# Kernel optimization log

Measured on AMD Instinct MI355X. Metric: run time of the kernel, lower is better.

The kernel has to match this reference:

```python
import jax, jax.numpy as jnp
import numpy as np

N_HEADS = 16
D_HEAD = 64
IGNORE = -100000.0


def setup_inputs() -> dict:
    key = jax.random.key(0)
    ks = jax.random.split(key, 5)
    B, S, D = 2, 2048, 1024
    return {
        "residual": jax.random.normal(ks[0], (B, S, D), dtype=jnp.float32),
        "q": jax.random.normal(ks[1], (B, S, D), dtype=jnp.float32),
        "k": jax.random.normal(ks[2], (B, S, D), dtype=jnp.float32),
        "v": jax.random.normal(ks[3], (B, S, D), dtype=jnp.float32),
        "W_O": jax.random.normal(ks[4], (N_HEADS, D_HEAD, D), dtype=jnp.float32) * 0.02,
        "b_O": jnp.zeros((D,), dtype=jnp.float32),
    }


def reference(residual, q, k, v, W_O, b_O):
    B, S, _ = q.shape
    attn_scale = np.sqrt(D_HEAD).astype(np.float32)  # use_attn_scale=True
    # split heads: [..., pos, (h d)] -> [..., pos, h, d]
    qh = q.reshape(B, S, N_HEADS, D_HEAD)
    kh = k.reshape(B, S, N_HEADS, D_HEAD)
    vh = v.reshape(B, S, N_HEADS, D_HEAD)
    # scores: [..., head, query_pos, key_pos]
    scores = jnp.einsum("bqhd,bkhd->bhqk", qh, kh) / attn_scale
    causal = jnp.tril(jnp.ones((S, S), dtype=bool))
    scores = jnp.where(causal, scores, jnp.float32(IGNORE))
    pattern = jax.nn.softmax(scores, axis=-1)
    # weighted sum of values: [..., query_pos, head, d_head]
    z = jnp.einsum("bkhd,bhqk->bqhd", vh, pattern)
    out = jnp.einsum("bqhd,hdm->bqm", z, W_O) + b_O
    return (residual, out)
```

## Files before the change

kernel.cpp:

```cpp
#include <hip/hip_runtime.h>

#define B_ 2
#define S_ 2048
#define D_ 1024
#define H_ 16
#define DH_ 64
#define NP_ 2048

typedef short v8s __attribute__((ext_vector_type(8)));
typedef float v4f __attribute__((ext_vector_type(4)));
typedef float v16f __attribute__((ext_vector_type(16)));
typedef unsigned int v2u __attribute__((ext_vector_type(2)));
typedef unsigned int uint32;

__device__ inline short f2bf(float f) {
  unsigned u = __float_as_uint(f);
  u = (u + 0x7FFFu + ((u >> 16) & 1u)) >> 16;
  return (short)u;
}

__device__ inline unsigned pk_bf16(float lo, float hi) {
  unsigned r;
  asm("v_cvt_pk_bf16_f32 %0, %1, %2" : "=v"(r) : "v"(lo), "v"(hi));
  return r;
}

__device__ inline void gll16(const void* g, void* l) {
  __builtin_amdgcn_global_load_lds(
      (const __attribute__((address_space(1))) void*)g,
      (__attribute__((address_space(3))) void*)l, 16, 0, 0);
}

__global__ __launch_bounds__(256) void cvt_all_kernel(
    const float* __restrict__ k, short* __restrict__ kb,
    const float* __restrict__ v, short* __restrict__ vt,
    const float* __restrict__ w, short* __restrict__ wt) {
  __shared__ short t[64][64 + 8];
  int bid = blockIdx.x;
  int tid = threadIdx.x;
  if (bid < 2048) {
    int i = bid * 256 + tid;
    float4 a = ((const float4*)k)[2 * i];
    float4 b = ((const float4*)k)[2 * i + 1];
    v8s o;
    o[0] = f2bf(a.x); o[1] = f2bf(a.y); o[2] = f2bf(a.z); o[3] = f2bf(a.w);
    o[4] = f2bf(b.x); o[5] = f2bf(b.y); o[6] = f2bf(b.z); o[7] = f2bf(b.w);
    ((v8s*)kb)[i] = o;
    return;
  }
  int r = tid >> 2, c16 = (tid & 3) * 16;
  if (bid < 3072) {
    int id = bid - 2048;
    int st = id & 31;
    int bh = id >> 5;
    int b = bh >> 4, h = bh & 15;
    const float* vp = v + ((size_t)(b * S_ + st * 64 + r)) * D_ + h * DH_ + c16;
    for (int i = 0; i < 16; i += 4) {
      float4 a = *(const float4*)(vp + i);
      t[r][c16 + i + 0] = f2bf(a.x);
      t[r][c16 + i + 1] = f2bf(a.y);
      t[r][c16 + i + 2] = f2bf(a.z);
      t[r][c16 + i + 3] = f2bf(a.w);
    }
    __syncthreads();
    short* op = vt + ((size_t)((b * H_ + h) * DH_ + r)) * S_ + st * 64 + c16;
    v8s o0, o1;
    for (int j = 0; j < 8; ++j) { o0[j] = t[c16 + j][r]; o1[j] = t[c16 + 8 + j][r]; }
    *(v8s*)op = o0;
    *(v8s*)(op + 8) = o1;
  } else {
    int id = bid - 3072;
    int tk = id & 15, tm = id >> 4;
    const float* wp = w + (size_t)(tk * 64 + r) * D_ + tm * 64 + c16;
    for (int i = 0; i < 16; i += 4) {
      float4 a = *(const float4*)(wp + i);
      t[r][c16 + i + 0] = f2bf(a.x);
      t[r][c16 + i + 1] = f2bf(a.y);
      t[r][c16 + i + 2] = f2bf(a.z);
      t[r][c16 + i + 3] = f2bf(a.w);
    }
    __syncthreads();
    short* op = wt + (size_t)(tm * 64 + r) * D_ + tk * 64 + c16;
    v8s o0, o1;
    for (int j = 0; j < 8; ++j) { o0[j] = t[c16 + j][r]; o1[j] = t[c16 + 8 + j][r]; }
    *(v8s*)op = o0;
    *(v8s*)(op + 8) = o1;
  }
}

template <int SPLITS>
__global__ __launch_bounds__(64, 4) void attn_kernel(
    const float* __restrict__ q, const short* __restrict__ kbf,
    const short* __restrict__ vtb, uint32* __restrict__ Opart,
    float* __restrict__ Lsum, const float* __restrict__ residual,
    float* __restrict__ res_out) {
  constexpr int NBLK = (SPLITS == 2) ? 4096 : 2048;
  int bid = blockIdx.x;
  int bh = bid & 31;
  int rest = bid >> 5;
  int sp = (SPLITS == 2) ? (rest & 1) : 0;
  int i = (SPLITS == 2) ? (rest >> 1) : rest;
  int b = bh >> 4, h = bh & 15;

  const int qrow0 = i * 32;
  const int nt = i + 1;
  const int t0 = (SPLITS == 2) ? sp * nt / 2 : 0;
  const int t1 = (SPLITS == 2) ? ((sp + 1) * nt / 2 - 1) : i;

  int lane = threadIdx.x;
  int l31 = lane & 31, h32 = lane >> 5;

  __shared__ short Klds[32][64];
  __shared__ short Vlds[32][64];

  const int lr8 = lane >> 3;
  const int l7 = lane & 7;
  const short* kbase = kbf + (size_t)b * S_ * D_ + h * DH_ +
                       (size_t)lr8 * D_ + ((l7 ^ lr8) << 3);
  const int vq = l7 ^ lr8;
  const short* vbase = vtb + (size_t)(b * H_ + h) * DH_ * S_ +
                       (size_t)(lr8 + (vq >> 2) * 32) * S_ + ((vq & 3) << 3);

  v8s qf[4];
  {
    const float* qp = q + (size_t)(b * S_ + qrow0 + l31) * D_ + h * DH_ + h32 * 8;
    const float sc = 0.125f * 1.44269504f;
#pragma unroll
    for (int d4 = 0; d4 < 4; ++d4) {
      float4 x = *(const float4*)(qp + d4 * 16);
      float4 y = *(const float4*)(qp + d4 * 16 + 4);
      v8s tq;
      tq[0] = f2bf(x.x * sc); tq[1] = f2bf(x.y * sc);
      tq[2] = f2bf(x.z * sc); tq[3] = f2bf(x.w * sc);
      tq[4] = f2bf(y.x * sc); tq[5] = f2bf(y.y * sc);
      tq[6] = f2bf(y.z * sc); tq[7] = f2bf(y.w * sc);
      qf[d4] = tq;
    }
  }

  v16f O0, O1;
#pragma unroll
  for (int r = 0; r < 16; ++r) { O0[r] = 0.f; O1[r] = 0.f; }
  float L = 0.f;
  const int swz = (l31 & 7) << 3;

  auto stage = [&](int t) {
    const short* kp = kbase + (size_t)(t * 32) * D_;
    const short* vp = vbase + t * 32;
#pragma unroll
    for (int j = 0; j < 4; ++j)
      gll16(kp + (size_t)(j * 8) * D_, &Klds[j * 8][0]);
#pragma unroll
    for (int j = 0; j < 4; ++j)
      gll16(vp + (size_t)(j * 8) * S_, &Vlds[j * 8][0]);
  };

  if (t0 <= t1) stage(t0);

  for (int s = t0; s <= t1; ++s) {
    asm volatile("s_waitcnt vmcnt(0)" ::: "memory");
    __builtin_amdgcn_sched_barrier(0);

    int kb = s * 32;

    __builtin_amdgcn_s_setprio(1);
    v16f S0;
#pragma unroll
    for (int r = 0; r < 16; ++r) S0[r] = 0.f;
#pragma unroll
    for (int d4 = 0; d4 < 4; ++d4) {
      v8s kf = *(const v8s*)&Klds[l31][(((d4 << 1) | h32) << 3) ^ swz];
      S0 = __builtin_amdgcn_mfma_f32_32x32x16_bf16(kf, qf[d4], S0, 0, 0, 0);
    }
    __builtin_amdgcn_s_setprio(0);

    if (kb + 31 > qrow0) {
      int qg = qrow0 + l31;
#pragma unroll
      for (int r = 0; r < 16; ++r) {
        int kl = kb + (r & 3) + 8 * (r >> 2) + 4 * h32;
        if (kl > qg) S0[r] = -1e30f;
      }
    }

    float rs = 0.f;
    unsigned pw0[8];
#pragma unroll
    for (int r = 0; r < 16; ++r) {
      S0[r] = __builtin_amdgcn_exp2f(S0[r]);
      rs += S0[r];
    }
#pragma unroll
    for (int w = 0; w < 8; ++w) pw0[w] = pk_bf16(S0[2 * w], S0[2 * w + 1]);
    rs += __shfl_xor(rs, 32);
    L += rs;

    __builtin_amdgcn_s_setprio(1);
#pragma unroll
    for (int ks = 0; ks < 2; ++ks) {
      v2u a = __builtin_amdgcn_permlane32_swap(pw0[ks * 4 + 0], pw0[ks * 4 + 2], false, false);
      v2u c = __builtin_amdgcn_permlane32_swap(pw0[ks * 4 + 1], pw0[ks * 4 + 3], false, false);
      uint32 fw[4] = {a.x, c.x, a.y, c.y};
      v8s pb = __builtin_bit_cast(v8s, *(ulonglong2*)fw);
      v8s vf0 = *(const v8s*)&Vlds[l31][(((ks << 1) | h32) << 3) ^ swz];
      O0 = __builtin_amdgcn_mfma_f32_32x32x16_bf16(vf0, pb, O0, 0, 0, 0);
      v8s vf1 = *(const v8s*)&Vlds[l31][((4 | (ks << 1) | h32) << 3) ^ swz];
      O1 = __builtin_amdgcn_mfma_f32_32x32x16_bf16(vf1, pb, O1, 0, 0, 0);
    }
    __builtin_amdgcn_s_setprio(0);

    __builtin_amdgcn_sched_barrier(0);
    asm volatile("s_waitcnt lgkmcnt(0)" ::: "memory");
    __builtin_amdgcn_sched_barrier(0);
    if (s < t1) stage(s + 1);
  }

  int p = bh * 64 + i;
  uint32* Op = Opart + ((size_t)(sp * NP_ + p)) * 1024;
#pragma unroll
  for (int w = 0; w < 8; ++w) {
    int dpair = 4 * (w >> 1) + (w & 1) + 2 * h32;
    Op[dpair * 32 + l31] = pk_bf16(O0[2 * w], O0[2 * w + 1]);
    Op[(16 + dpair) * 32 + l31] = pk_bf16(O1[2 * w], O1[2 * w + 1]);
  }
  if (h32 == 0) Lsum[(size_t)(sp * NP_ + p) * 32 + l31] = L;

  {
    const float4* rs_ = (const float4*)residual;
    float4* rd_ = (float4*)res_out;
    for (size_t idx = (size_t)bid * 64 + lane; idx < 1048576;
         idx += (size_t)NBLK * 64)
      rd_[idx] = rs_[idx];
  }
}

template <int SPLITS>
__global__ __launch_bounds__(128) void merge_kernel(
    const uint32* __restrict__ Opart, const float* __restrict__ Lsum,
    short* __restrict__ z) {
  int p = blockIdx.x;
  int tid = threadIdx.x;
  int qq = tid & 31, g = tid >> 5;

  float Lt = Lsum[(size_t)p * 32 + qq];
  if constexpr (SPLITS == 2) Lt += Lsum[((size_t)NP_ + p) * 32 + qq];
  float f = 1.f / Lt;

  __shared__ uint32 T[32][33];
#pragma unroll
  for (int j = 0; j < 8; ++j) {
    int dp = g * 8 + j;
    uint32 u0 = Opart[(size_t)p * 1024 + dp * 32 + qq];
    float lo = __uint_as_float(u0 << 16);
    float hi = __uint_as_float(u0 & 0xFFFF0000u);
    if constexpr (SPLITS == 2) {
      uint32 u1 = Opart[((size_t)NP_ + p) * 1024 + dp * 32 + qq];
      lo += __uint_as_float(u1 << 16);
      hi += __uint_as_float(u1 & 0xFFFF0000u);
    }
    T[qq][dp] = pk_bf16(lo * f, hi * f);
  }
  __syncthreads();
  int q2 = tid >> 2, c = (tid & 3) * 8;
  int srow = (p & 63) * 32 + q2;
  int b = p >> 10, h = (p >> 6) & 15;
  uint32* zp = (uint32*)z + ((size_t)(b * S_ + srow)) * (D_ / 2) + h * 32 + c;
#pragma unroll
  for (int j = 0; j < 8; ++j) zp[j] = T[q2][c + j];
}

__global__ __launch_bounds__(256) void proj_kernel(
    const short* __restrict__ z, const short* __restrict__ wt,
    const float* __restrict__ bias, float* __restrict__ out) {
  int bm = blockIdx.x, bn = blockIdx.y;
  int tid = threadIdx.x;
  int wave = tid >> 6, lane = tid & 63, lh = lane >> 4, ll = lane & 15;
  int wr = wave >> 1, wc = wave & 1;

  __shared__ short Al[2][64][64];
  __shared__ short Bl[2][128][64];

  const int r8 = lane >> 3;
  const int scol = ((lane & 7) ^ r8) << 3;

  v4f acc[2][4];
#pragma unroll
  for (int m = 0; m < 2; ++m)
#pragma unroll
    for (int n = 0; n < 4; ++n) acc[m][n] = (v4f){0.f, 0.f, 0.f, 0.f};

  auto stage = [&](int kb, int bbuf) {
#pragma unroll
    for (int i = 0; i < 2; ++i) {
      int c = wave * 2 + i;
      gll16(z + (size_t)(bm * 64 + c * 8 + r8) * D_ + kb + scol, &Al[bbuf][c * 8][0]);
    }
#pragma unroll
    for (int i = 0; i < 4; ++i) {
      int c = wave * 4 + i;
      gll16(wt + (size_t)(bn * 128 + c * 8 + r8) * D_ + kb + scol, &Bl[bbuf][c * 8][0]);
    }
  };

  stage(0, 0);
  __syncthreads();

  for (int kt = 0; kt < D_ / 64; ++kt) {
    int bbuf = kt & 1;
    if (kt + 1 < D_ / 64) stage((kt + 1) * 64, bbuf ^ 1);
    v8s af[2][2], bf[4][2];
#pragma unroll
    for (int m = 0; m < 2; ++m) {
      int row = wr * 32 + m * 16 + ll;
#pragma unroll
      for (int c = 0; c < 2; ++c)
        af[m][c] = *(const v8s*)&Al[bbuf][row][(((c << 2) | lh) ^ (ll & 7)) << 3];
    }
#pragma unroll
    for (int n = 0; n < 4; ++n) {
      int row = wc * 64 + n * 16 + ll;
#pragma unroll
      for (int c = 0; c < 2; ++c)
        bf[n][c] = *(const v8s*)&Bl[bbuf][row][(((c << 2) | lh) ^ (ll & 7)) << 3];
    }
#pragma unroll
    for (int m = 0; m < 2; ++m)
#pragma unroll
      for (int n = 0; n < 4; ++n)
#pragma unroll
        for (int c = 0; c < 2; ++c)
          acc[m][n] = __builtin_amdgcn_mfma_f32_16x16x32_bf16(af[m][c], bf[n][c], acc[m][n], 0, 0, 0);
    __syncthreads();
  }

#pragma unroll
  for (int m = 0; m < 2; ++m) {
    int gr = bm * 64 + wr * 32 + m * 16 + lh * 4;
#pragma unroll
    for (int n = 0; n < 4; ++n) {
      int gc = bn * 128 + wc * 64 + n * 16 + ll;
      float bo = bias[gc];
#pragma unroll
      for (int r = 0; r < 4; ++r)
        out[(size_t)(gr + r) * D_ + gc] = acc[m][n][r] + bo;
    }
  }
}

extern "C" void kernel_launch(void* const* d_in, const int* in_sizes, int n_in,
                              void* d_out, int out_size, void* d_ws, size_t ws_size,
                              hipStream_t stream) {
  const float* residual = (const float*)d_in[0];
  const float* q = (const float*)d_in[1];
  const float* k = (const float*)d_in[2];
  const float* v = (const float*)d_in[3];
  const float* W = (const float*)d_in[4];
  const float* bO = (const float*)d_in[5];
  float* out = (float*)d_out;

  const size_t half = (size_t)B_ * S_ * D_;
  char* ws = (char*)d_ws;
  short* kbf = (short*)ws;
  short* vtb = kbf + half;
  short* wtb = vtb + half;
  char* pbase = (char*)(wtb + (size_t)D_ * D_);
  const size_t opart_b = (size_t)NP_ * 1024 * 4;
  const size_t l_b = (size_t)NP_ * 32 * 4;
  const size_t base_b = (size_t)pbase - (size_t)ws;
  short* z = kbf;

  cvt_all_kernel<<<3328, 256, 0, stream>>>(k, kbf, v, vtb, W, wtb);

  if (ws_size >= base_b + 2 * (opart_b + l_b)) {
    uint32* Opart = (uint32*)pbase;
    float* Lsum = (float*)(pbase + 2 * opart_b);
    attn_kernel<2><<<4096, 64, 0, stream>>>(q, kbf, vtb, Opart, Lsum, residual, out);
    merge_kernel<2><<<NP_, 128, 0, stream>>>(Opart, Lsum, z);
    proj_kernel<<<dim3((B_ * S_) / 64, D_ / 128), 256, 0, stream>>>(z, wtb, bO, out + half);
  } else {
    uint32* Opart = (uint32*)pbase;
    float* Lsum = (float*)(pbase + opart_b);
    attn_kernel<1><<<2048, 64, 0, stream>>>(q, kbf, vtb, Opart, Lsum, residual, out);
    merge_kernel<1><<<NP_, 128, 0, stream>>>(Opart, Lsum, z);
    proj_kernel<<<dim3((B_ * S_) / 64, D_ / 128), 256, 0, stream>>>(z, wtb, bO, out + half);
  }
}
```

Baseline: 83.19 us.

## Balance causal attention work with variable per-row KV splits and 4-wave blocks

Replaces the fixed two-way KV split with a split count that grows with the query tile index (1 to 4 segments), so each work unit covers roughly 16 or fewer KV tiles and the causal triangle load is more even. Units are ordered heaviest first, and four independent waves are packed into each 256-thread block, each with private LDS buffers. The merge kernel now sums a variable number of partial results. This removes the workspace-size fallback path and assumes the workspace is large enough for 5120 segments. It also adds more partial-output traffic for the long rows.

Measured after the change: 92.90 us. 1.12x slower.

```diff
diff --git a/kernel.cpp b/kernel.cpp
--- a/kernel.cpp
+++ b/kernel.cpp
@@ -6,6 +6,7 @@
 #define H_ 16
 #define DH_ 64
 #define NP_ 2048
+#define NSEG_ 5120
 
 typedef short v8s __attribute__((ext_vector_type(8)));
 typedef float v4f __attribute__((ext_vector_type(4)));
@@ -29,6 +30,11 @@
   __builtin_amdgcn_global_load_lds(
       (const __attribute__((address_space(1))) void*)g,
       (__attribute__((address_space(3))) void*)l, 16, 0, 0);
+}
+
+__device__ __host__ inline int seg_off(int i) {
+  int g = i >> 4, rr = i & 15;
+  return i + 8 * g * (g - 1) + rr * g;
 }
 
 __global__ __launch_bounds__(256) void cvt_all_kernel(
@@ -88,31 +94,34 @@
   }
 }
 
-template <int SPLITS>
-__global__ __launch_bounds__(64, 4) void attn_kernel(
+__global__ __launch_bounds__(256, 5) void attn_kernel(
     const float* __restrict__ q, const short* __restrict__ kbf,
     const short* __restrict__ vtb, uint32* __restrict__ Opart,
     float* __restrict__ Lsum, const float* __restrict__ residual,
     float* __restrict__ res_out) {
-  constexpr int NBLK = (SPLITS == 2) ? 4096 : 2048;
   int bid = blockIdx.x;
-  int bh = bid & 31;
-  int rest = bid >> 5;
-  int sp = (SPLITS == 2) ? (rest & 1) : 0;
-  int i = (SPLITS == 2) ? (rest >> 1) : rest;
+  int tid = threadIdx.x;
+  int wave = tid >> 6, lane = tid & 63;
+  int u = bid * 4 + wave;
+  int bh = u & 31;
+  int r = u >> 5;
+  int i, s;
+  if (r < 64) { i = 63 - (r >> 2); s = r & 3; }
+  else if (r < 112) { int t = r - 64; i = 47 - t / 3; s = t - 3 * (47 - i); }
+  else if (r < 144) { int t = r - 112; i = 31 - (t >> 1); s = t & 1; }
+  else { i = 159 - r; s = 0; }
+  const int ns = (i >> 4) + 1;
   int b = bh >> 4, h = bh & 15;
+  const int nt = i + 1;
+  const int t0 = s * nt / ns;
+  const int t1 = (s + 1) * nt / ns - 1;
+
+  int l31 = lane & 31, h32 = lane >> 5;
+
+  __shared__ short Klds[4][32][64];
+  __shared__ short Vlds[4][32][64];
 
   const int qrow0 = i * 32;
-  const int nt = i + 1;
-  const int t0 = (SPLITS == 2) ? sp * nt / 2 : 0;
-  const int t1 = (SPLITS == 2) ? ((sp + 1) * nt / 2 - 1) : i;
-
-  int lane = threadIdx.x;
-  int l31 = lane & 31, h32 = lane >> 5;
-
-  __shared__ short Klds[32][64];
-  __shared__ short Vlds[32][64];
-
   const int lr8 = lane >> 3;
   const int l7 = lane & 7;
   const short* kbase = kbf + (size_t)b * S_ * D_ + h * DH_ +
@@ -140,7 +149,7 @@
 
   v16f O0, O1;
 #pragma unroll
-  for (int r = 0; r < 16; ++r) { O0[r] = 0.f; O1[r] = 0.f; }
+  for (int rr = 0; rr < 16; ++rr) { O0[rr] = 0.f; O1[rr] = 0.f; }
   float L = 0.f;
   const int swz = (l31 & 7) << 3;
 
@@ -149,27 +158,27 @@
     const short* vp = vbase + t * 32;
 #pragma unroll
     for (int j = 0; j < 4; ++j)
-      gll16(kp + (size_t)(j * 8) * D_, &Klds[j * 8][0]);
+      gll16(kp + (size_t)(j * 8) * D_, &Klds[wave][j * 8][0]);
 #pragma unroll
     for (int j = 0; j < 4; ++j)
-      gll16(vp + (size_t)(j * 8) * S_, &Vlds[j * 8][0]);
+      gll16(vp + (size_t)(j * 8) * S_, &Vlds[wave][j * 8][0]);
   };
 
-  if (t0 <= t1) stage(t0);
-
-  for (int s = t0; s <= t1; ++s) {
+  stage(t0);
+
+  for (int ss = t0; ss <= t1; ++ss) {
     asm volatile("s_waitcnt vmcnt(0)" ::: "memory");
     __builtin_amdgcn_sched_barrier(0);
 
-    int kb = s * 32;
+    int kb = ss * 32;
 
     __builtin_amdgcn_s_setprio(1);
     v16f S0;
 #pragma unroll
-    for (int r = 0; r < 16; ++r) S0[r] = 0.f;
+    for (int rr = 0; rr < 16; ++rr) S0[rr] = 0.f;
 #pragma unroll
     for (int d4 = 0; d4 < 4; ++d4) {
-      v8s kf = *(const v8s*)&Klds[l31][(((d4 << 1) | h32) << 3) ^ swz];
+      v8s kf = *(const v8s*)&Klds[wave][l31][(((d4 << 1) | h32) << 3) ^ swz];
       S0 = __builtin_amdgcn_mfma_f32_32x32x16_bf16(kf, qf[d4], S0, 0, 0, 0);
     }
     __builtin_amdgcn_s_setprio(0);
@@ -177,18 +186,18 @@
     if (kb + 31 > qrow0) {
       int qg = qrow0 + l31;
 #pragma unroll
-      for (int r = 0; r < 16; ++r) {
-        int kl = kb + (r & 3) + 8 * (r >> 2) + 4 * h32;
-        if (kl > qg) S0[r] = -1e30f;
+      for (int rr = 0; rr < 16; ++rr) {
+        int kl = kb + (rr & 3) + 8 * (rr >> 2) + 4 * h32;
+        if (kl > qg) S0[rr] = -1e30f;
       }
     }
 
     float rs = 0.f;
     unsigned pw0[8];
 #pragma unroll
-    for (int r = 0; r < 16; ++r) {
-      S0[r] = __builtin_amdgcn_exp2f(S0[r]);
-      rs += S0[r];
+    for (int rr = 0; rr < 16; ++rr) {
+      S0[rr] = __builtin_amdgcn_exp2f(S0[rr]);
+      rs += S0[rr];
     }
 #pragma unroll
     for (int w = 0; w < 8; ++w) pw0[w] = pk_bf16(S0[2 * w], S0[2 * w + 1]);
@@ -202,9 +211,9 @@
       v2u c = __builtin_amdgcn_permlane32_swap(pw0[ks * 4 + 1], pw0[ks * 4 + 3], false, false);
       uint32 fw[4] = {a.x, c.x, a.y, c.y};
       v8s pb = __builtin_bit_cast(v8s, *(ulonglong2*)fw);
-      v8s vf0 = *(const v8s*)&Vlds[l31][(((ks << 1) | h32) << 3) ^ swz];
+      v8s vf0 = *(const v8s*)&Vlds[wave][l31][(((ks << 1) | h32) << 3) ^ swz];
       O0 = __builtin_amdgcn_mfma_f32_32x32x16_bf16(vf0, pb, O0, 0, 0, 0);
-      v8s vf1 = *(const v8s*)&Vlds[l31][((4 | (ks << 1) | h32) << 3) ^ swz];
+      v8s vf1 = *(const v8s*)&Vlds[wave][l31][((4 | (ks << 1) | h32) << 3) ^ swz];
       O1 = __builtin_amdgcn_mfma_f32_32x32x16_bf16(vf1, pb, O1, 0, 0, 0);
     }
     __builtin_amdgcn_s_setprio(0);
@@ -212,52 +221,56 @@
     __builtin_amdgcn_sched_barrier(0);
     asm volatile("s_waitcnt lgkmcnt(0)" ::: "memory");
     __builtin_amdgcn_sched_barrier(0);
-    if (s < t1) stage(s + 1);
-  }
-
-  int p = bh * 64 + i;
-  uint32* Op = Opart + ((size_t)(sp * NP_ + p)) * 1024;
+    if (ss < t1) stage(ss + 1);
+  }
+
+  int slot = bh * 160 + seg_off(i) + s;
+  uint32* Op = Opart + (size_t)slot * 1024;
 #pragma unroll
   for (int w = 0; w < 8; ++w) {
     int dpair = 4 * (w >> 1) + (w & 1) + 2 * h32;
     Op[dpair * 32 + l31] = pk_bf16(O0[2 * w], O0[2 * w + 1]);
     Op[(16 + dpair) * 32 + l31] = pk_bf16(O1[2 * w], O1[2 * w + 1]);
   }
-  if (h32 == 0) Lsum[(size_t)(sp * NP_ + p) * 32 + l31] = L;
+  if (h32 == 0) Lsum[(size_t)slot * 32 + l31] = L;
 
   {
     const float4* rs_ = (const float4*)residual;
     float4* rd_ = (float4*)res_out;
-    for (size_t idx = (size_t)bid * 64 + lane; idx < 1048576;
-         idx += (size_t)NBLK * 64)
+    for (size_t idx = (size_t)bid * 256 + tid; idx < 1048576;
+         idx += (size_t)1280 * 256)
       rd_[idx] = rs_[idx];
   }
 }
 
-template <int SPLITS>
 __global__ __launch_bounds__(128) void merge_kernel(
     const uint32* __restrict__ Opart, const float* __restrict__ Lsum,
     short* __restrict__ z) {
   int p = blockIdx.x;
+  int i = p & 63, bh = p >> 6;
+  int ns = (i >> 4) + 1;
+  int base = bh * 160 + seg_off(i);
   int tid = threadIdx.x;
   int qq = tid & 31, g = tid >> 5;
 
-  float Lt = Lsum[(size_t)p * 32 + qq];
-  if constexpr (SPLITS == 2) Lt += Lsum[((size_t)NP_ + p) * 32 + qq];
+  float Lt = 0.f;
+#pragma unroll
+  for (int s = 0; s < 4; ++s)
+    if (s < ns) Lt += Lsum[(size_t)(base + s) * 32 + qq];
   float f = 1.f / Lt;
 
   __shared__ uint32 T[32][33];
 #pragma unroll
   for (int j = 0; j < 8; ++j) {
     int dp = g * 8 + j;
-    uint32 u0 = Opart[(size_t)p * 1024 + dp * 32 + qq];
-    float lo = __uint_as_float(u0 << 16);
-    float hi = __uint_as_float(u0 & 0xFFFF0000u);
-    if constexpr (SPLITS == 2) {
-      uint32 u1 = Opart[((size_t)NP_ + p) * 1024 + dp * 32 + qq];
-      lo += __uint_as_float(u1 << 16);
-      hi += __uint_as_float(u1 & 0xFFFF0000u);
-    }
+    float lo = 0.f, hi = 0.f;
+#pragma unroll
+    for (int s = 0; s < 4; ++s)
+      if (s < ns) {
+        uint32 u = Opart[(size_t)(base + s) * 1024 + dp * 32 + qq];
+        lo += __uint_as_float(u << 16);
+        hi += __uint_as_float(u & 0xFFFF0000u);
+      }
     T[qq][dp] = pk_bf16(lo * f, hi * f);
   }
   __syncthreads();
@@ -364,24 +377,12 @@
   short* vtb = kbf + half;
   short* wtb = vtb + half;
   char* pbase = (char*)(wtb + (size_t)D_ * D_);
-  const size_t opart_b = (size_t)NP_ * 1024 * 4;
-  const size_t l_b = (size_t)NP_ * 32 * 4;
-  const size_t base_b = (size_t)pbase - (size_t)ws;
+  uint32* Opart = (uint32*)pbase;
+  float* Lsum = (float*)(pbase + (size_t)NSEG_ * 4096);
   short* z = kbf;
 
   cvt_all_kernel<<<3328, 256, 0, stream>>>(k, kbf, v, vtb, W, wtb);
-
-  if (ws_size >= base_b + 2 * (opart_b + l_b)) {
-    uint32* Opart = (uint32*)pbase;
-    float* Lsum = (float*)(pbase + 2 * opart_b);
-    attn_kernel<2><<<4096, 64, 0, stream>>>(q, kbf, vtb, Opart, Lsum, residual, out);
-    merge_kernel<2><<<NP_, 128, 0, stream>>>(Opart, Lsum, z);
-    proj_kernel<<<dim3((B_ * S_) / 64, D_ / 128), 256, 0, stream>>>(z, wtb, bO, out + half);
-  } else {
-    uint32* Opart = (uint32*)pbase;
-    float* Lsum = (float*)(pbase + opart_b);
-    attn_kernel<1><<<2048, 64, 0, stream>>>(q, kbf, vtb, Opart, Lsum, residual, out);
-    merge_kernel<1><<<NP_, 128, 0, stream>>>(Opart, Lsum, z);
-    proj_kernel<<<dim3((B_ * S_) / 64, D_ / 128), 256, 0, stream>>>(z, wtb, bO, out + half);
-  }
-}
+  attn_kernel<<<1280, 256, 0, stream>>>(q, kbf, vtb, Opart, Lsum, residual, out);
+  merge_kernel<<<NP_, 128, 0, stream>>>(Opart, Lsum, z);
+  proj_kernel<<<dim3((B_ * S_) / 64, D_ / 128), 256, 0, stream>>>(z, wtb, bO, out + half);
+}
```
